# Performance work log

Hardware: AMD Instinct MI355X
Metric: run time of the kernel (lower is better)

The kernel has to match this reference:

```python
import jax, jax.numpy as jnp
from jax import lax
import numpy as np

SEQ, BATCH, IN, H = 512, 8192, 2, 10


def setup_inputs() -> dict:
    key = jax.random.key(0)
    ks = jax.random.split(key, 11)
    s = 1.0 / np.sqrt(H)  # torch default uniform(-1/sqrt(H), 1/sqrt(H))
    u = lambda k, shp: jax.random.uniform(k, shp, jnp.float32, -s, s)
    return {
        "x": jax.random.normal(ks[0], (SEQ, BATCH, IN), jnp.float32),
        "w_ih0": u(ks[1], (4 * H, IN)),
        "w_hh0": u(ks[2], (4 * H, H)),
        "b_ih0": u(ks[3], (4 * H,)),
        "b_hh0": u(ks[4], (4 * H,)),
        "w_ih1": u(ks[5], (4 * H, H)),
        "w_hh1": u(ks[6], (4 * H, H)),
        "b_ih1": u(ks[7], (4 * H,)),
        "b_hh1": u(ks[8], (4 * H,)),
        "fc_w": u(ks[9], (2, H)),
        "fc_b": u(ks[10], (2,)),
    }


def _lstm_layer(x, w_ih, w_hh, b_ih, b_hh):
    # x: [T, B, in]; torch gate order: i, f, g, o
    B = x.shape[1]
    # precompute input projections for all timesteps: [T, B, 4H]
    xg = jnp.einsum("tbi,gi->tbg", x, w_ih) + b_ih + b_hh

    def step(carry, xt):
        h, c = carry
        gates = xt + h @ w_hh.T  # [B, 4H]
        i, f, g, o = jnp.split(gates, 4, axis=-1)
        i = jax.nn.sigmoid(i)
        f = jax.nn.sigmoid(f)
        g = jnp.tanh(g)
        o = jax.nn.sigmoid(o)
        c = f * c + i * g
        h = o * jnp.tanh(c)
        return (h, c), h

    h0 = jnp.zeros((B, H), x.dtype)
    _, ys = lax.scan(step, (h0, h0), xg)
    return ys  # [T, B, H]


def reference(x, w_ih0, w_hh0, b_ih0, b_hh0, w_ih1, w_hh1, b_ih1, b_hh1, fc_w, fc_b):
    h1 = _lstm_layer(x, w_ih0, w_hh0, b_ih0, b_hh0)
    h2 = _lstm_layer(h1, w_ih1, w_hh1, b_ih1, b_hh1)
    last = h2[-1]  # [B, H]
    return last @ fc_w.T + fc_b  # [B, 2]
```

## Files before the change

kernel.cpp:

```cpp
#include <hip/hip_runtime.h>

#define SEQ 512
#define BATCH 8192
#define LOG2E  1.44269504088896340736f
#define LOG2E2 2.88539008177792681472f

typedef _Float16 f16x8 __attribute__((ext_vector_type(8)));
typedef float    f32x4 __attribute__((ext_vector_type(4)));

__device__ __forceinline__ float fexp2(float x) { return __builtin_amdgcn_exp2f(x); }
__device__ __forceinline__ float frcp(float x)  { return __builtin_amdgcn_rcpf(x); }

__global__ __launch_bounds__(64) void lstm2_fc_mfma(
    const float* __restrict__ x,
    const float* __restrict__ w_ih0, const float* __restrict__ w_hh0,
    const float* __restrict__ b_ih0, const float* __restrict__ b_hh0,
    const float* __restrict__ w_ih1, const float* __restrict__ w_hh1,
    const float* __restrict__ b_ih1, const float* __restrict__ b_hh1,
    const float* __restrict__ fc_w, const float* __restrict__ fc_b,
    float* __restrict__ out)
{
    __shared__ float hfc[16][10];

    const int lane = threadIdx.x;
    const int e    = lane & 15;
    const int q    = lane >> 4;
    const int Eb   = blockIdx.x * 16;
    const bool qz  = (q == 0);

    f16x8 ahi[5], alo[5];
    f32x4 cb[5];
    bool  l1p[5];
    #pragma unroll
    for (int T = 0; T < 5; ++T) {
        const int Pa = 4 * T + (e >> 2), Ga = e & 3;
        const int La = (Pa >= 10);
        const int Ua = Pa - La * 10;
        const int wr = Ga * 10 + Ua;
        const float m = (Ga == 2) ? LOG2E2 : -LOG2E;
        #pragma unroll
        for (int j = 0; j < 8; ++j) {
            const int k = q * 8 + j;
            float w = 0.0f;
            if (k < 2) {
                w = La ? 0.0f : w_ih0[wr * 2 + k];
            } else if (j >= 2 && j <= 6) {
                const int p = 4 * (j - 2) + q;
                if (p < 10) w = La ? w_ih1[wr * 10 + p] : w_hh0[wr * 10 + p];
                else        w = La ? w_hh1[wr * 10 + (p - 10)] : 0.0f;
            }
            const float wm = m * w;
            const _Float16 wh = (_Float16)wm;
            ahi[T][j] = wh;
            alo[T][j] = (_Float16)(wm - (float)wh);
        }
        const int Pc = 4 * T + q;
        l1p[T] = (Pc >= 10);
        const int Lc = (Pc >= 10);
        const int Uc = Pc - Lc * 10;
        #pragma unroll
        for (int r = 0; r < 4; ++r) {
            const int wrc = r * 10 + Uc;
            const float mc = (r == 2) ? LOG2E2 : -LOG2E;
            cb[T][r] = mc * (Lc ? (b_ih1[wrc] + b_hh1[wrc])
                                : (b_ih0[wrc] + b_hh0[wrc]));
        }
    }

    f16x8 bh, bl;
    #pragma unroll
    for (int j = 0; j < 8; ++j) { bh[j] = (_Float16)0.f; bl[j] = (_Float16)0.f; }

    const float* xe = x + ((size_t)Eb + e) * 2;
    const float2 x0 = *(const float2*)xe;
    const float2 x1 = *(const float2*)(xe + (size_t)1 * BATCH * 2);
    float2 xr0[8], xr1[8];
    #pragma unroll
    for (int i = 0; i < 8; ++i) xr0[i] = *(const float2*)(xe + (size_t)(2 + i) * BATCH * 2);
    #pragma unroll
    for (int i = 0; i < 8; ++i) xr1[i] = *(const float2*)(xe + (size_t)(10 + i) * BATCH * 2);

    {
        const _Float16 xa = (_Float16)x0.x, xb2 = (_Float16)x0.y;
        bh[0] = qz ? xa : (_Float16)0.f;
        bh[1] = qz ? xb2 : (_Float16)0.f;
        bl[0] = qz ? (_Float16)(x0.x - (float)xa) : (_Float16)0.f;
        bl[1] = qz ? (_Float16)(x0.y - (float)xb2) : (_Float16)0.f;
    }

    float cst[5] = {0.f, 0.f, 0.f, 0.f, 0.f};
    float hT[5];

#define ACT(T, ZZ, SUP)                                                        \
    {                                                                          \
        const float d0 = 1.0f + fexp2(ZZ[0]);                                  \
        const float d1 = 1.0f + fexp2(ZZ[1]);                                  \
        const float d2 = 1.0f + fexp2(ZZ[2]);                                  \
        const float d3 = 1.0f + fexp2(ZZ[3]);                                  \
        const float m1 = d0 * d1, m2 = d2 * d3;                                \
        const float pq_ = frcp(m1 * m2);                                       \
        const float pif = m2 * pq_, pgo = m1 * pq_;                            \
        const float si = d1 * pif, sf = d0 * pif;                              \
        const float tg = fmaf(-2.0f, d3 * pgo, 1.0f);                          \
        sO[T] = d2 * pgo;                                                      \
        float cn = fmaf(sf, cst[T], si * tg);                                  \
        if (SUP) cn = l1p[T] ? 0.0f : cn;       \
        cst[T] = cn;                                                           \
        eC[T] = 1.0f + fexp2(LOG2E2 * cn);                                     \
    }

#define STEP(XIN, SUP)                                                         \
    {                                                                          \
        f32x4 z0 = __builtin_amdgcn_mfma_f32_16x16x32_f16(ahi[0], bh, cb[0], 0, 0, 0); \
        f32x4 z1 = __builtin_amdgcn_mfma_f32_16x16x32_f16(ahi[1], bh, cb[1], 0, 0, 0); \
        f32x4 z2 = __builtin_amdgcn_mfma_f32_16x16x32_f16(ahi[2], bh, cb[2], 0, 0, 0); \
        f32x4 z3 = __builtin_amdgcn_mfma_f32_16x16x32_f16(ahi[3], bh, cb[3], 0, 0, 0); \
        f32x4 z4 = __builtin_amdgcn_mfma_f32_16x16x32_f16(ahi[4], bh, cb[4], 0, 0, 0); \
        z0 = __builtin_amdgcn_mfma_f32_16x16x32_f16(alo[0], bh, z0, 0, 0, 0);  \
        z1 = __builtin_amdgcn_mfma_f32_16x16x32_f16(alo[1], bh, z1, 0, 0, 0);  \
        z2 = __builtin_amdgcn_mfma_f32_16x16x32_f16(alo[2], bh, z2, 0, 0, 0);  \
        z3 = __builtin_amdgcn_mfma_f32_16x16x32_f16(alo[3], bh, z3, 0, 0, 0);  \
        z4 = __builtin_amdgcn_mfma_f32_16x16x32_f16(alo[4], bh, z4, 0, 0, 0);  \
        z0 = __builtin_amdgcn_mfma_f32_16x16x32_f16(ahi[0], bl, z0, 0, 0, 0);  \
        z1 = __builtin_amdgcn_mfma_f32_16x16x32_f16(ahi[1], bl, z1, 0, 0, 0);  \
        z2 = __builtin_amdgcn_mfma_f32_16x16x32_f16(ahi[2], bl, z2, 0, 0, 0);  \
        z3 = __builtin_amdgcn_mfma_f32_16x16x32_f16(ahi[3], bl, z3, 0, 0, 0);  \
        z4 = __builtin_amdgcn_mfma_f32_16x16x32_f16(ahi[4], bl, z4, 0, 0, 0);  \
        float eC[5], sO[5];                                                    \
        ACT(0, z0, SUP) ACT(1, z1, SUP) ACT(2, z2, SUP)                        \
        ACT(3, z3, SUP) ACT(4, z4, SUP)                                        \
        const float p01 = frcp(eC[0] * eC[1]);                                 \
        const float p23 = frcp(eC[2] * eC[3]);                                 \
        const float p4  = frcp(eC[4]);                                         \
        hT[0] = sO[0] * fmaf(-2.0f, eC[1] * p01, 1.0f);                        \
        hT[1] = sO[1] * fmaf(-2.0f, eC[0] * p01, 1.0f);                        \
        hT[2] = sO[2] * fmaf(-2.0f, eC[3] * p23, 1.0f);                        \
        hT[3] = sO[3] * fmaf(-2.0f, eC[2] * p23, 1.0f);                        \
        hT[4] = sO[4] * fmaf(-2.0f, p4, 1.0f);                                 \
        _Pragma("unroll")                                                      \
        for (int T = 0; T < 5; ++T) {                                          \
            const _Float16 hh = (_Float16)hT[T];                               \
            bh[2 + T] = hh;                                                    \
            bl[2 + T] = (_Float16)(hT[T] - (float)hh);                         \
        }                                                                      \
        const _Float16 xa = (_Float16)(XIN).x, xb2 = (_Float16)(XIN).y;        \
        bh[0] = qz ? xa : (_Float16)0.f;                                       \
        bh[1] = qz ? xb2 : (_Float16)0.f;                                      \
        bl[0] = qz ? (_Float16)((XIN).x - (float)xa) : (_Float16)0.f;          \
        bl[1] = qz ? (_Float16)((XIN).y - (float)xb2) : (_Float16)0.f;         \
    }

    STEP(x1, 1)

    for (int cc = 0; cc < 32; ++cc) {
        #pragma unroll
        for (int s = 0; s < 8; ++s) STEP(xr0[s], 0)
        #pragma unroll
        for (int i = 0; i < 8; ++i) {
            int ti = 16 * cc + 18 + i; if (ti > 511) ti = 511;
            xr0[i] = *(const float2*)(xe + (size_t)ti * BATCH * 2);
        }
        #pragma unroll
        for (int s = 0; s < 8; ++s) STEP(xr1[s], 0)
        #pragma unroll
        for (int i = 0; i < 8; ++i) {
            int ti = 16 * cc + 26 + i; if (ti > 511) ti = 511;
            xr1[i] = *(const float2*)(xe + (size_t)ti * BATCH * 2);
        }
    }
#undef STEP
#undef ACT

    if (q >= 2) hfc[e][q - 2] = hT[2];
    hfc[e][2 + q] = hT[3];
    hfc[e][6 + q] = hT[4];
    __syncthreads();
    if (lane < 32) {
        const int ee = lane >> 1, jj = lane & 1;
        float acc = fc_b[jj];
        #pragma unroll
        for (int u = 0; u < 10; ++u)
            acc = fmaf(fc_w[jj * 10 + u], hfc[ee][u], acc);
        out[((size_t)Eb + ee) * 2 + jj] = acc;
    }
}

extern "C" void kernel_launch(void* const* d_in, const int* in_sizes, int n_in,
                              void* d_out, int out_size, void* d_ws, size_t ws_size,
                              hipStream_t stream) {
    const float* x     = (const float*)d_in[0];
    const float* w_ih0 = (const float*)d_in[1];
    const float* w_hh0 = (const float*)d_in[2];
    const float* b_ih0 = (const float*)d_in[3];
    const float* b_hh0 = (const float*)d_in[4];
    const float* w_ih1 = (const float*)d_in[5];
    const float* w_hh1 = (const float*)d_in[6];
    const float* b_ih1 = (const float*)d_in[7];
    const float* b_hh1 = (const float*)d_in[8];
    const float* fc_w  = (const float*)d_in[9];
    const float* fc_b  = (const float*)d_in[10];
    float* out = (float*)d_out;

    const int threads = 64;
    const int blocks  = BATCH / 16;
    lstm2_fc_mfma<<<blocks, threads, 0, stream>>>(
        x, w_ih0, w_hh0, b_ih0, b_hh0,
        w_ih1, w_hh1, b_ih1, b_hh1, fc_w, fc_b, out);
}
```

Before: 226.6 us.

## Split LSTM layers across two wavefronts with LDS mailbox handoff

Each block now runs two wavefronts: wave 0 computes layer 0 and wave 1 computes layer 1, one timestep behind. Layer-0 hidden states pass through a double-buffered LDS mailbox as packed hi/lo fp16 pairs. This halves the MFMA and activation work per wave on the serial critical path (three tiles instead of five) and lets the two layers run concurrently. The cost is a block-wide barrier every timestep plus LDS traffic, and twice as many waves per block.

```diff
diff --git a/kernel.cpp b/kernel.cpp
--- a/kernel.cpp
+++ b/kernel.cpp
@@ -11,7 +11,7 @@
 __device__ __forceinline__ float fexp2(float x) { return __builtin_amdgcn_exp2f(x); }
 __device__ __forceinline__ float frcp(float x)  { return __builtin_amdgcn_rcpf(x); }
 
-__global__ __launch_bounds__(64) void lstm2_fc_mfma(
+__global__ __launch_bounds__(128) void lstm2_fc_mfma(
     const float* __restrict__ x,
     const float* __restrict__ w_ih0, const float* __restrict__ w_hh0,
     const float* __restrict__ b_ih0, const float* __restrict__ b_hh0,
@@ -20,34 +20,37 @@
     const float* __restrict__ fc_w, const float* __restrict__ fc_b,
     float* __restrict__ out)
 {
+    __shared__ unsigned mbox[2][3][64];
     __shared__ float hfc[16][10];
 
-    const int lane = threadIdx.x;
+    const int tid  = threadIdx.x;
+    const int w1   = tid >> 6;
+    const int lane = tid & 63;
     const int e    = lane & 15;
     const int q    = lane >> 4;
     const int Eb   = blockIdx.x * 16;
     const bool qz  = (q == 0);
 
-    f16x8 ahi[5], alo[5];
-    f32x4 cb[5];
-    bool  l1p[5];
+    f16x8 ahi[3], alo[3];
+    f32x4 cb[3];
     #pragma unroll
-    for (int T = 0; T < 5; ++T) {
+    for (int T = 0; T < 3; ++T) {
         const int Pa = 4 * T + (e >> 2), Ga = e & 3;
-        const int La = (Pa >= 10);
-        const int Ua = Pa - La * 10;
-        const int wr = Ga * 10 + Ua;
-        const float m = (Ga == 2) ? LOG2E2 : -LOG2E;
+        const bool realA = (Pa < 10);
+        const int wr = Ga * 10 + (realA ? Pa : 0);
+        const float m = ((Ga == 2) ? LOG2E2 : -LOG2E) * (realA ? 1.0f : 0.0f);
         #pragma unroll
         for (int j = 0; j < 8; ++j) {
-            const int k = q * 8 + j;
             float w = 0.0f;
-            if (k < 2) {
-                w = La ? 0.0f : w_ih0[wr * 2 + k];
-            } else if (j >= 2 && j <= 6) {
-                const int p = 4 * (j - 2) + q;
-                if (p < 10) w = La ? w_ih1[wr * 10 + p] : w_hh0[wr * 10 + p];
-                else        w = La ? w_hh1[wr * 10 + (p - 10)] : 0.0f;
+            if (!w1) {
+                if (j < 2)      { if (q == 0) w = w_ih0[wr * 2 + j]; }
+                else if (j < 5) { const int u = 4 * (j - 2) + q;
+                                  if (u < 10) w = w_hh0[wr * 10 + u]; }
+            } else {
+                if (j < 3)      { const int u = 4 * j + q;
+                                  if (u < 10) w = w_ih1[wr * 10 + u]; }
+                else if (j < 6) { const int u = 4 * (j - 3) + q;
+                                  if (u < 10) w = w_hh1[wr * 10 + u]; }
             }
             const float wm = m * w;
             const _Float16 wh = (_Float16)wm;
@@ -55,43 +58,41 @@
             alo[T][j] = (_Float16)(wm - (float)wh);
         }
         const int Pc = 4 * T + q;
-        l1p[T] = (Pc >= 10);
-        const int Lc = (Pc >= 10);
-        const int Uc = Pc - Lc * 10;
+        const bool realC = (Pc < 10);
         #pragma unroll
         for (int r = 0; r < 4; ++r) {
-            const int wrc = r * 10 + Uc;
-            const float mc = (r == 2) ? LOG2E2 : -LOG2E;
-            cb[T][r] = mc * (Lc ? (b_ih1[wrc] + b_hh1[wrc])
+            const int wrc = r * 10 + (realC ? Pc : 0);
+            const float mc = ((r == 2) ? LOG2E2 : -LOG2E) * (realC ? 1.0f : 0.0f);
+            cb[T][r] = mc * (w1 ? (b_ih1[wrc] + b_hh1[wrc])
                                 : (b_ih0[wrc] + b_hh0[wrc]));
         }
     }
 
-    f16x8 bh, bl;
+    f16x8 Bh, Bl;
     #pragma unroll
-    for (int j = 0; j < 8; ++j) { bh[j] = (_Float16)0.f; bl[j] = (_Float16)0.f; }
+    for (int j = 0; j < 8; ++j) { Bh[j] = (_Float16)0.f; Bl[j] = (_Float16)0.f; }
 
     const float* xe = x + ((size_t)Eb + e) * 2;
-    const float2 x0 = *(const float2*)xe;
-    const float2 x1 = *(const float2*)(xe + (size_t)1 * BATCH * 2);
+    float2 x1v{0.f, 0.f};
     float2 xr0[8], xr1[8];
-    #pragma unroll
-    for (int i = 0; i < 8; ++i) xr0[i] = *(const float2*)(xe + (size_t)(2 + i) * BATCH * 2);
-    #pragma unroll
-    for (int i = 0; i < 8; ++i) xr1[i] = *(const float2*)(xe + (size_t)(10 + i) * BATCH * 2);
-
-    {
+    if (!w1) {
+        const float2 x0 = *(const float2*)xe;
+        x1v = *(const float2*)(xe + (size_t)1 * BATCH * 2);
+        #pragma unroll
+        for (int i = 0; i < 8; ++i) xr0[i] = *(const float2*)(xe + (size_t)(2 + i) * BATCH * 2);
+        #pragma unroll
+        for (int i = 0; i < 8; ++i) xr1[i] = *(const float2*)(xe + (size_t)(10 + i) * BATCH * 2);
         const _Float16 xa = (_Float16)x0.x, xb2 = (_Float16)x0.y;
-        bh[0] = qz ? xa : (_Float16)0.f;
-        bh[1] = qz ? xb2 : (_Float16)0.f;
-        bl[0] = qz ? (_Float16)(x0.x - (float)xa) : (_Float16)0.f;
-        bl[1] = qz ? (_Float16)(x0.y - (float)xb2) : (_Float16)0.f;
-    }
-
-    float cst[5] = {0.f, 0.f, 0.f, 0.f, 0.f};
-    float hT[5];
-
-#define ACT(T, ZZ, SUP)                                                        \
+        Bh[0] = qz ? xa : (_Float16)0.f;
+        Bh[1] = qz ? xb2 : (_Float16)0.f;
+        Bl[0] = qz ? (_Float16)(x0.x - (float)xa) : (_Float16)0.f;
+        Bl[1] = qz ? (_Float16)(x0.y - (float)xb2) : (_Float16)0.f;
+    }
+
+    float cst[3] = {0.f, 0.f, 0.f};
+    float hT[3];
+
+#define ACT(T, ZZ)                                                             \
     {                                                                          \
         const float d0 = 1.0f + fexp2(ZZ[0]);                                  \
         const float d1 = 1.0f + fexp2(ZZ[1]);                                  \
@@ -103,80 +104,111 @@
         const float si = d1 * pif, sf = d0 * pif;                              \
         const float tg = fmaf(-2.0f, d3 * pgo, 1.0f);                          \
         sO[T] = d2 * pgo;                                                      \
-        float cn = fmaf(sf, cst[T], si * tg);                                  \
-        if (SUP) cn = l1p[T] ? 0.0f : cn;       \
-        cst[T] = cn;                                                           \
-        eC[T] = 1.0f + fexp2(LOG2E2 * cn);                                     \
-    }
-
-#define STEP(XIN, SUP)                                                         \
-    {                                                                          \
-        f32x4 z0 = __builtin_amdgcn_mfma_f32_16x16x32_f16(ahi[0], bh, cb[0], 0, 0, 0); \
-        f32x4 z1 = __builtin_amdgcn_mfma_f32_16x16x32_f16(ahi[1], bh, cb[1], 0, 0, 0); \
-        f32x4 z2 = __builtin_amdgcn_mfma_f32_16x16x32_f16(ahi[2], bh, cb[2], 0, 0, 0); \
-        f32x4 z3 = __builtin_amdgcn_mfma_f32_16x16x32_f16(ahi[3], bh, cb[3], 0, 0, 0); \
-        f32x4 z4 = __builtin_amdgcn_mfma_f32_16x16x32_f16(ahi[4], bh, cb[4], 0, 0, 0); \
-        z0 = __builtin_amdgcn_mfma_f32_16x16x32_f16(alo[0], bh, z0, 0, 0, 0);  \
-        z1 = __builtin_amdgcn_mfma_f32_16x16x32_f16(alo[1], bh, z1, 0, 0, 0);  \
-        z2 = __builtin_amdgcn_mfma_f32_16x16x32_f16(alo[2], bh, z2, 0, 0, 0);  \
-        z3 = __builtin_amdgcn_mfma_f32_16x16x32_f16(alo[3], bh, z3, 0, 0, 0);  \
-        z4 = __builtin_amdgcn_mfma_f32_16x16x32_f16(alo[4], bh, z4, 0, 0, 0);  \
-        z0 = __builtin_amdgcn_mfma_f32_16x16x32_f16(ahi[0], bl, z0, 0, 0, 0);  \
-        z1 = __builtin_amdgcn_mfma_f32_16x16x32_f16(ahi[1], bl, z1, 0, 0, 0);  \
-        z2 = __builtin_amdgcn_mfma_f32_16x16x32_f16(ahi[2], bl, z2, 0, 0, 0);  \
-        z3 = __builtin_amdgcn_mfma_f32_16x16x32_f16(ahi[3], bl, z3, 0, 0, 0);  \
-        z4 = __builtin_amdgcn_mfma_f32_16x16x32_f16(ahi[4], bl, z4, 0, 0, 0);  \
-        float eC[5], sO[5];                                                    \
-        ACT(0, z0, SUP) ACT(1, z1, SUP) ACT(2, z2, SUP)                        \
-        ACT(3, z3, SUP) ACT(4, z4, SUP)                                        \
+        cst[T] = fmaf(sf, cst[T], si * tg);                                    \
+        eC[T] = 1.0f + fexp2(LOG2E2 * cst[T]);                                 \
+    }
+
+#define MFMA9()                                                                \
+        f32x4 z0 = __builtin_amdgcn_mfma_f32_16x16x32_f16(ahi[0], Bh, cb[0], 0, 0, 0); \
+        f32x4 z1 = __builtin_amdgcn_mfma_f32_16x16x32_f16(ahi[1], Bh, cb[1], 0, 0, 0); \
+        f32x4 z2 = __builtin_amdgcn_mfma_f32_16x16x32_f16(ahi[2], Bh, cb[2], 0, 0, 0); \
+        z0 = __builtin_amdgcn_mfma_f32_16x16x32_f16(alo[0], Bh, z0, 0, 0, 0);  \
+        z1 = __builtin_amdgcn_mfma_f32_16x16x32_f16(alo[1], Bh, z1, 0, 0, 0);  \
+        z2 = __builtin_amdgcn_mfma_f32_16x16x32_f16(alo[2], Bh, z2, 0, 0, 0);  \
+        z0 = __builtin_amdgcn_mfma_f32_16x16x32_f16(ahi[0], Bl, z0, 0, 0, 0);  \
+        z1 = __builtin_amdgcn_mfma_f32_16x16x32_f16(ahi[1], Bl, z1, 0, 0, 0);  \
+        z2 = __builtin_amdgcn_mfma_f32_16x16x32_f16(ahi[2], Bl, z2, 0, 0, 0);  \
+        float eC[3], sO[3];                                                    \
+        ACT(0, z0) ACT(1, z1) ACT(2, z2)                                       \
         const float p01 = frcp(eC[0] * eC[1]);                                 \
-        const float p23 = frcp(eC[2] * eC[3]);                                 \
-        const float p4  = frcp(eC[4]);                                         \
+        const float p2  = frcp(eC[2]);                                         \
         hT[0] = sO[0] * fmaf(-2.0f, eC[1] * p01, 1.0f);                        \
         hT[1] = sO[1] * fmaf(-2.0f, eC[0] * p01, 1.0f);                        \
-        hT[2] = sO[2] * fmaf(-2.0f, eC[3] * p23, 1.0f);                        \
-        hT[3] = sO[3] * fmaf(-2.0f, eC[2] * p23, 1.0f);                        \
-        hT[4] = sO[4] * fmaf(-2.0f, p4, 1.0f);                                 \
+        hT[2] = sO[2] * fmaf(-2.0f, p2, 1.0f);
+
+#define STEP0(XIN, MBUF)                                                       \
+    {                                                                          \
+        MFMA9()                                                                \
         _Pragma("unroll")                                                      \
-        for (int T = 0; T < 5; ++T) {                                          \
+        for (int T = 0; T < 3; ++T) {                                          \
             const _Float16 hh = (_Float16)hT[T];                               \
-            bh[2 + T] = hh;                                                    \
-            bl[2 + T] = (_Float16)(hT[T] - (float)hh);                         \
+            const _Float16 hl = (_Float16)(hT[T] - (float)hh);                 \
+            Bh[2 + T] = hh;                                                    \
+            Bl[2 + T] = hl;                                                    \
+            mbox[MBUF][T][lane] =                                              \
+                (unsigned)__builtin_bit_cast(unsigned short, hh) |             \
+                ((unsigned)__builtin_bit_cast(unsigned short, hl) << 16);      \
         }                                                                      \
         const _Float16 xa = (_Float16)(XIN).x, xb2 = (_Float16)(XIN).y;        \
-        bh[0] = qz ? xa : (_Float16)0.f;                                       \
-        bh[1] = qz ? xb2 : (_Float16)0.f;                                      \
-        bl[0] = qz ? (_Float16)((XIN).x - (float)xa) : (_Float16)0.f;          \
-        bl[1] = qz ? (_Float16)((XIN).y - (float)xb2) : (_Float16)0.f;         \
-    }
-
-    STEP(x1, 1)
+        Bh[0] = qz ? xa : (_Float16)0.f;                                       \
+        Bh[1] = qz ? xb2 : (_Float16)0.f;                                      \
+        Bl[0] = qz ? (_Float16)((XIN).x - (float)xa) : (_Float16)0.f;          \
+        Bl[1] = qz ? (_Float16)((XIN).y - (float)xb2) : (_Float16)0.f;         \
+    }
+
+#define STEP1(MBUF)                                                            \
+    {                                                                          \
+        _Pragma("unroll")                                                      \
+        for (int T = 0; T < 3; ++T) {                                          \
+            const unsigned mv = mbox[MBUF][T][lane];                           \
+            Bh[T] = __builtin_bit_cast(_Float16, (unsigned short)(mv & 0xffffu)); \
+            Bl[T] = __builtin_bit_cast(_Float16, (unsigned short)(mv >> 16));  \
+        }                                                                      \
+        MFMA9()                                                                \
+        _Pragma("unroll")                                                      \
+        for (int T = 0; T < 3; ++T) {                                          \
+            const _Float16 hh = (_Float16)hT[T];                               \
+            Bh[3 + T] = hh;                                                    \
+            Bl[3 + T] = (_Float16)(hT[T] - (float)hh);                         \
+        }                                                                      \
+    }
+
+    if (!w1) STEP0(x1v, 0)
+    __syncthreads();
 
     for (int cc = 0; cc < 32; ++cc) {
         #pragma unroll
-        for (int s = 0; s < 8; ++s) STEP(xr0[s], 0)
-        #pragma unroll
-        for (int i = 0; i < 8; ++i) {
-            int ti = 16 * cc + 18 + i; if (ti > 511) ti = 511;
-            xr0[i] = *(const float2*)(xe + (size_t)ti * BATCH * 2);
+        for (int s = 0; s < 16; ++s) {
+            const int wb = (s + 1) & 1;
+            const int rb = s & 1;
+            if (!w1) {
+                if (cc < 31 || s < 15) {
+                    const float2 xin = (s < 8) ? xr0[s & 7] : xr1[s & 7];
+                    STEP0(xin, wb)
+                }
+            } else {
+                STEP1(rb)
+            }
+            __syncthreads();
+            if (!w1 && s == 7) {
+                #pragma unroll
+                for (int i = 0; i < 8; ++i) {
+                    int ti = 16 * cc + 18 + i; if (ti > 511) ti = 511;
+                    xr0[i] = *(const float2*)(xe + (size_t)ti * BATCH * 2);
+                }
+            }
+            if (!w1 && s == 15) {
+                #pragma unroll
+                for (int i = 0; i < 8; ++i) {
+                    int ti = 16 * cc + 26 + i; if (ti > 511) ti = 511;
+                    xr1[i] = *(const float2*)(xe + (size_t)ti * BATCH * 2);
+                }
+            }
         }
-        #pragma unroll
-        for (int s = 0; s < 8; ++s) STEP(xr1[s], 0)
-        #pragma unroll
-        for (int i = 0; i < 8; ++i) {
-            int ti = 16 * cc + 26 + i; if (ti > 511) ti = 511;
-            xr1[i] = *(const float2*)(xe + (size_t)ti * BATCH * 2);
-        }
-    }
-#undef STEP
+    }
+#undef STEP0
+#undef STEP1
+#undef MFMA9
 #undef ACT
 
-    if (q >= 2) hfc[e][q - 2] = hT[2];
-    hfc[e][2 + q] = hT[3];
-    hfc[e][6 + q] = hT[4];
+    if (w1) {
+        hfc[e][q]     = hT[0];
+        hfc[e][4 + q] = hT[1];
+        if (q < 2) hfc[e][8 + q] = hT[2];
+    }
     __syncthreads();
-    if (lane < 32) {
-        const int ee = lane >> 1, jj = lane & 1;
+    if (tid < 32) {
+        const int ee = tid >> 1, jj = tid & 1;
         float acc = fc_b[jj];
         #pragma unroll
         for (int u = 0; u < 10; ++u)
@@ -201,7 +233,7 @@
     const float* fc_b  = (const float*)d_in[10];
     float* out = (float*)d_out;
 
-    const int threads = 64;
+    const int threads = 128;
     const int blocks  = BATCH / 16;
     lstm2_fc_mfma<<<blocks, threads, 0, stream>>>(
         x, w_ih0, w_hh0, b_ih0, b_hh0,
```

Result: slower. 319.1 us (+40.8%).
